# Kernel optimization log

Hardware: AMD Instinct MI355X
Metric: run time of the kernel (lower is better)

Reference implementation:

```python
import jax, jax.numpy as jnp
import numpy as np

E = 2048  # embedding_size; must equal seq_len for the original assignment to be shape-valid
B = 64    # batch


def setup_inputs() -> dict:
    key = jax.random.key(0)
    # tokens must lie in dictionary = {1, ..., E-1}; otherwise the original code drops rows
    x = jax.random.randint(key, (B, E), 1, E, dtype=jnp.int32)
    return {"x": x}


def reference(x):
    # Original per-token encoding: (m-1) leading '0's + bin(v) + trailing '1'
    # == big-endian E-bit binary representation of (2*v + 1).
    # Due to the transposed slice assignment, Y[j, b, i] = bit (E-1-b) of (2*x[i,j]+1).
    v = (2 * x + 1).astype(jnp.int32)                     # [B, J]
    shifts = E - 1 - jnp.arange(E, dtype=jnp.int32)       # bit index for output column b
    safe = jnp.minimum(shifts, 31)                        # v is nonneg, so v>>31 == 0 (correct high bits)
    bits = (v[:, :, None] >> safe[None, None, :]) & 1     # [B, J, E]
    return jnp.transpose(bits, (1, 2, 0)).astype(jnp.float32)  # Y: [J, E, B] == [seq, emb, batch]
```

## Files before the change

kernel.cpp:

```cpp
#include <hip/hip_runtime.h>


#define EMB 2048
#define BATCH 64

__global__ __launch_bounds__(256) void emb_bits_kernel(
    const int* __restrict__ x, float4* __restrict__ out) {
    unsigned int q  = blockIdx.x * 256u + threadIdx.x;
    unsigned int i4 = q & 15u;
    unsigned int jb = q >> 4;
    unsigned int b  = jb & 2047u;
    unsigned int j  = jb >> 11;
    int shift = 2047 - (int)b;

    float4 val = make_float4(0.f, 0.f, 0.f, 0.f);
    if (shift <= 11) {
        unsigned int i0 = i4 * 4u;
        int v0 = 2 * x[(i0 + 0) * EMB + j] + 1;
        int v1 = 2 * x[(i0 + 1) * EMB + j] + 1;
        int v2 = 2 * x[(i0 + 2) * EMB + j] + 1;
        int v3 = 2 * x[(i0 + 3) * EMB + j] + 1;
        val.x = (float)((v0 >> shift) & 1);
        val.y = (float)((v1 >> shift) & 1);
        val.z = (float)((v2 >> shift) & 1);
        val.w = (float)((v3 >> shift) & 1);
    }
    out[q] = val;
}

extern "C" void kernel_launch(void* const* d_in, const int* in_sizes, int n_in,
                              void* d_out, int out_size, void* d_ws, size_t ws_size,
                              hipStream_t stream) {
    const int* x = (const int*)d_in[0];
    float4* out = (float4*)d_out;
    const unsigned int quads = (unsigned int)EMB * EMB * BATCH / 4u;
    dim3 grid(quads / 256u);
    emb_bits_kernel<<<grid, dim3(256), 0, stream>>>(x, out);
}
```

Baseline: 1.023 ms.

## Use one block per sequence position with nontemporal zero stores

After: 1.035 ms. About the same (+1.1%).

```diff
diff --git a/kernel.cpp b/kernel.cpp
--- a/kernel.cpp
+++ b/kernel.cpp
@@ -3,37 +3,45 @@
 
 #define EMB 2048
 #define BATCH 64
+#define QUADS_PER_J (EMB * BATCH / 4)
+#define NITER (QUADS_PER_J / 256)
+
+typedef float floatx4 __attribute__((ext_vector_type(4)));
 
 __global__ __launch_bounds__(256) void emb_bits_kernel(
-    const int* __restrict__ x, float4* __restrict__ out) {
-    unsigned int q  = blockIdx.x * 256u + threadIdx.x;
-    unsigned int i4 = q & 15u;
-    unsigned int jb = q >> 4;
-    unsigned int b  = jb & 2047u;
-    unsigned int j  = jb >> 11;
-    int shift = 2047 - (int)b;
+    const int* __restrict__ x, floatx4* __restrict__ out) {
+    const unsigned int j = blockIdx.x;
+    const unsigned int t = threadIdx.x;
+    floatx4* __restrict__ base = out + (size_t)j * QUADS_PER_J + t;
 
-    float4 val = make_float4(0.f, 0.f, 0.f, 0.f);
-    if (shift <= 11) {
-        unsigned int i0 = i4 * 4u;
-        int v0 = 2 * x[(i0 + 0) * EMB + j] + 1;
-        int v1 = 2 * x[(i0 + 1) * EMB + j] + 1;
-        int v2 = 2 * x[(i0 + 2) * EMB + j] + 1;
-        int v3 = 2 * x[(i0 + 3) * EMB + j] + 1;
+    const floatx4 zero = (floatx4)(0.f);
+
+    #pragma unroll 4
+    for (int it = 0; it < NITER - 1; ++it) {
+        __builtin_nontemporal_store(zero, base + (size_t)it * 256u);
+    }
+
+    floatx4 val = zero;
+    const unsigned int brow = t >> 4;
+    if (brow >= 4u) {
+        const int shift = 15 - (int)brow;
+        const unsigned int i0 = (t & 15u) * 4u;
+        const int v0 = 2 * x[(i0 + 0u) * EMB + j] + 1;
+        const int v1 = 2 * x[(i0 + 1u) * EMB + j] + 1;
+        const int v2 = 2 * x[(i0 + 2u) * EMB + j] + 1;
+        const int v3 = 2 * x[(i0 + 3u) * EMB + j] + 1;
         val.x = (float)((v0 >> shift) & 1);
         val.y = (float)((v1 >> shift) & 1);
         val.z = (float)((v2 >> shift) & 1);
         val.w = (float)((v3 >> shift) & 1);
     }
-    out[q] = val;
+    __builtin_nontemporal_store(val, base + (size_t)(NITER - 1) * 256u);
 }
 
 extern "C" void kernel_launch(void* const* d_in, const int* in_sizes, int n_in,
                               void* d_out, int out_size, void* d_ws, size_t ws_size,
                               hipStream_t stream) {
     const int* x = (const int*)d_in[0];
-    float4* out = (float4*)d_out;
-    const unsigned int quads = (unsigned int)EMB * EMB * BATCH / 4u;
-    dim3 grid(quads / 256u);
-    emb_bits_kernel<<<grid, dim3(256), 0, stream>>>(x, out);
+    floatx4* out = (floatx4*)d_out;
+    emb_bits_kernel<<<dim3(EMB), dim3(256), 0, stream>>>(x, out);
 }
```
